# Kernel tuning notes

Measured on AMD Instinct MI355X. Metric: run time of the kernel, lower is better.

Reference implementation:

```python
import jax, jax.numpy as jnp
import numpy as np

N_NODES = 50000
N_EDGES = 1600000
IN_DIM = 128
HEADS = 4
HID = 16
NEG_SLOPE = 0.2  # DGL GATConv default


def setup_inputs() -> dict:
    key = jax.random.key(0)
    ks = jax.random.split(key, 7)
    features = jax.random.normal(ks[0], (N_NODES, IN_DIM), dtype=jnp.float32)
    W = jax.random.normal(ks[1], (IN_DIM, HEADS * HID), dtype=jnp.float32) * 0.1
    attn_l = jax.random.normal(ks[2], (HEADS, HID), dtype=jnp.float32) * 0.1
    attn_r = jax.random.normal(ks[3], (HEADS, HID), dtype=jnp.float32) * 0.1
    bias = jax.random.normal(ks[4], (HEADS * HID,), dtype=jnp.float32) * 0.1
    src = jax.random.randint(ks[5], (N_EDGES,), 0, N_NODES, dtype=jnp.int64)
    dst = jax.random.randint(ks[6], (N_EDGES,), 0, N_NODES, dtype=jnp.int64)
    return {"features": features, "W": W, "attn_l": attn_l, "attn_r": attn_r,
            "bias": bias, "src": src, "dst": dst}


def reference(features, W, attn_l, attn_r, bias, src, dst):
    N = features.shape[0]
    H, D = attn_l.shape
    # linear projection -> per-head features [N, H, D]
    feat = (features @ W).reshape(N, H, D)
    el = jnp.einsum('nhd,hd->nh', feat, attn_l)  # [N, H]
    er = jnp.einsum('nhd,hd->nh', feat, attn_r)  # [N, H]
    # per-edge unnormalized attention logits [E, H]
    e = jax.nn.leaky_relu(el[src] + er[dst], negative_slope=NEG_SLOPE)
    # edge softmax segmented by destination node (numerically stable)
    emax = jax.ops.segment_max(e, dst, num_segments=N)
    ee = jnp.exp(e - emax[dst])
    denom = jax.ops.segment_sum(ee, dst, num_segments=N)
    alpha = ee / denom[dst]  # [E, H]
    # weighted neighbor aggregation: scatter-add of alpha * feat[src]
    msg = feat[src] * alpha[:, :, None]  # [E, H, D]
    out = jax.ops.segment_sum(msg, dst, num_segments=N)  # [N, H, D]
    out = out + bias.reshape(1, H, D)
    # wrapper GAT.forward averages over heads
    return out.mean(axis=1)  # [N, D]
```

## Files before the change

### kernel.cpp

```cpp
#include <hip/hip_runtime.h>
#include <hip/hip_bf16.h>

#define IN_DIM 128
#define HEADS 4
#define HID 16
#define HD 64
#define NEG_SLOPE 0.2f
#define PSHIFT 7
#define PCAP 5120
#define NPMAX 512
#define EPB 4096

typedef __attribute__((ext_vector_type(8))) short bf16x8;
typedef __attribute__((ext_vector_type(4))) float f32x4;

__device__ __forceinline__ float lrelu_exp(float x) {
    float e = x > 0.0f ? x : NEG_SLOPE * x;
    return __expf(e);
}

__device__ __forceinline__ unsigned short f2bf(float x) {
    unsigned int u = __float_as_uint(x);
    return (unsigned short)((u + 0x7fffu + ((u >> 16) & 1u)) >> 16);
}

__global__ __launch_bounds__(256) void k_project(const float* __restrict__ features,
                                                 const float* __restrict__ W,
                                                 const float* __restrict__ attn_l,
                                                 const float* __restrict__ attn_r,
                                                 __hip_bfloat16* __restrict__ feat16,
                                                 float* __restrict__ el,
                                                 float* __restrict__ er,
                                                 int* __restrict__ cursor,
                                                 int n_nodes, int npart) {
    if (blockIdx.x == 0) {
        for (int i = threadIdx.x; i < npart; i += 256) cursor[i] = 0;
    }
    __shared__ float Wl[IN_DIM * HD];
    for (int i = threadIdx.x; i < IN_DIM * HD; i += 256) Wl[i] = W[i];
    __syncthreads();

    const int lane  = threadIdx.x & 63;
    const int wave  = threadIdx.x >> 6;
    const int colid = lane & 15;
    const int quad  = lane >> 4;

    float al[4], ar[4];
#pragma unroll
    for (int c = 0; c < 4; ++c) {
        al[c] = attn_l[c * 16 + colid];
        ar[c] = attn_r[c * 16 + colid];
    }

    bf16x8 bf[16];
#pragma unroll
    for (int c = 0; c < 4; ++c) {
#pragma unroll
        for (int q = 0; q < 4; ++q) {
            bf16x8 v;
#pragma unroll
            for (int j = 0; j < 8; ++j) {
                int k = q * 32 + quad * 8 + j;
                v[j] = (short)f2bf(Wl[k * HD + c * 16 + colid]);
            }
            bf[c * 4 + q] = v;
        }
    }

    const int ngroups = (n_nodes + 15) >> 4;
    const int gwave = blockIdx.x * 4 + wave;
    const int nwaves = gridDim.x * 4;

    for (int g = gwave; g < ngroups; g += nwaves) {
        const int n0 = g * 16;
        int rown = n0 + colid;
        if (rown >= n_nodes) rown = n_nodes - 1;
        const float* fp = features + (size_t)rown * IN_DIM + quad * 8;

        f32x4 acc0 = {0.f, 0.f, 0.f, 0.f};
        f32x4 acc1 = {0.f, 0.f, 0.f, 0.f};
        f32x4 acc2 = {0.f, 0.f, 0.f, 0.f};
        f32x4 acc3 = {0.f, 0.f, 0.f, 0.f};
#pragma unroll
        for (int q = 0; q < 4; ++q) {
            float4 a0 = *reinterpret_cast<const float4*>(fp + q * 32);
            float4 a1 = *reinterpret_cast<const float4*>(fp + q * 32 + 4);
            bf16x8 av;
            av[0] = (short)f2bf(a0.x); av[1] = (short)f2bf(a0.y);
            av[2] = (short)f2bf(a0.z); av[3] = (short)f2bf(a0.w);
            av[4] = (short)f2bf(a1.x); av[5] = (short)f2bf(a1.y);
            av[6] = (short)f2bf(a1.z); av[7] = (short)f2bf(a1.w);
            acc0 = __builtin_amdgcn_mfma_f32_16x16x32_bf16(av, bf[0 * 4 + q], acc0, 0, 0, 0);
            acc1 = __builtin_amdgcn_mfma_f32_16x16x32_bf16(av, bf[1 * 4 + q], acc1, 0, 0, 0);
            acc2 = __builtin_amdgcn_mfma_f32_16x16x32_bf16(av, bf[2 * 4 + q], acc2, 0, 0, 0);
            acc3 = __builtin_amdgcn_mfma_f32_16x16x32_bf16(av, bf[3 * 4 + q], acc3, 0, 0, 0);
        }

        f32x4 accs[4] = {acc0, acc1, acc2, acc3};
        const bool full = (n0 + 16 <= n_nodes);
#pragma unroll
        for (int c = 0; c < 4; ++c) {
            f32x4 v = accs[c];
#pragma unroll
            for (int r = 0; r < 4; ++r) {
                int n = n0 + quad * 4 + r;
                if (full || n < n_nodes) {
                    ((unsigned short*)feat16)[(size_t)n * HD + c * 16 + colid] = f2bf(v[r]);
                }
            }
            float pl0 = v[0] * al[c], pl1 = v[1] * al[c], pl2 = v[2] * al[c], pl3 = v[3] * al[c];
            float pr0 = v[0] * ar[c], pr1 = v[1] * ar[c], pr2 = v[2] * ar[c], pr3 = v[3] * ar[c];
#pragma unroll
            for (int m = 1; m < 16; m <<= 1) {
                pl0 += __shfl_xor(pl0, m); pl1 += __shfl_xor(pl1, m);
                pl2 += __shfl_xor(pl2, m); pl3 += __shfl_xor(pl3, m);
                pr0 += __shfl_xor(pr0, m); pr1 += __shfl_xor(pr1, m);
                pr2 += __shfl_xor(pr2, m); pr3 += __shfl_xor(pr3, m);
            }
            if (colid == 0) {
                int nb = n0 + quad * 4;
                if (full) {
                    el[(size_t)(nb + 0) * HEADS + c] = pl0;
                    el[(size_t)(nb + 1) * HEADS + c] = pl1;
                    el[(size_t)(nb + 2) * HEADS + c] = pl2;
                    el[(size_t)(nb + 3) * HEADS + c] = pl3;
                    er[(size_t)(nb + 0) * HEADS + c] = pr0;
                    er[(size_t)(nb + 1) * HEADS + c] = pr1;
                    er[(size_t)(nb + 2) * HEADS + c] = pr2;
                    er[(size_t)(nb + 3) * HEADS + c] = pr3;
                } else {
                    float pls[4] = {pl0, pl1, pl2, pl3};
                    float prs[4] = {pr0, pr1, pr2, pr3};
                    for (int r = 0; r < 4; ++r) {
                        if (nb + r < n_nodes) {
                            el[(size_t)(nb + r) * HEADS + c] = pls[r];
                            er[(size_t)(nb + r) * HEADS + c] = prs[r];
                        }
                    }
                }
            }
        }
    }
}

__global__ __launch_bounds__(256) void k_partition(const int* __restrict__ src,
                                                   const int* __restrict__ dst,
                                                   int* __restrict__ cursor,
                                                   unsigned int* __restrict__ partbuf,
                                                   int n_edges, int npart) {
    __shared__ int hist[NPMAX];
    __shared__ int base[NPMAX];
    const int t = threadIdx.x;
    for (int i = t; i < npart; i += 256) hist[i] = 0;
    __syncthreads();

    const int e0 = blockIdx.x * EPB;
    unsigned int vals[16];
#pragma unroll
    for (int j = 0; j < 4; ++j) {
        int e = e0 + j * 1024 + t * 4;
        if (e + 4 <= n_edges) {
            int4 s4 = *reinterpret_cast<const int4*>(src + e);
            int4 d4 = *reinterpret_cast<const int4*>(dst + e);
            vals[j * 4 + 0] = ((unsigned)d4.x << 16) | (unsigned)s4.x;
            vals[j * 4 + 1] = ((unsigned)d4.y << 16) | (unsigned)s4.y;
            vals[j * 4 + 2] = ((unsigned)d4.z << 16) | (unsigned)s4.z;
            vals[j * 4 + 3] = ((unsigned)d4.w << 16) | (unsigned)s4.w;
        } else {
#pragma unroll
            for (int k = 0; k < 4; ++k) {
                int ee = e + k;
                vals[j * 4 + k] = (ee < n_edges)
                    ? (((unsigned)dst[ee] << 16) | (unsigned)src[ee])
                    : 0xffffffffu;
            }
        }
    }
#pragma unroll
    for (int j = 0; j < 16; ++j)
        if (vals[j] != 0xffffffffu) atomicAdd(&hist[vals[j] >> (16 + PSHIFT)], 1);
    __syncthreads();
    for (int i = t; i < npart; i += 256) {
        base[i] = atomicAdd(&cursor[i], hist[i]);
        hist[i] = 0;
    }
    __syncthreads();
#pragma unroll
    for (int j = 0; j < 16; ++j) {
        unsigned int v = vals[j];
        if (v != 0xffffffffu) {
            int p = v >> (16 + PSHIFT);
            int idx = base[p] + atomicAdd(&hist[p], 1);
            if (idx < PCAP) partbuf[(size_t)p * PCAP + idx] = v;
        }
    }
}

__global__ __launch_bounds__(256) void k_sort(const unsigned int* __restrict__ partbuf,
                                              const int* __restrict__ cursor,
                                              unsigned short* __restrict__ csr,
                                              int* __restrict__ row_ptr,
                                              unsigned short* __restrict__ deg16,
                                              int n_nodes) {
    __shared__ int hist[128];
    __shared__ int scan_s[128];
    const int p = blockIdx.x;
    const int t = threadIdx.x;
    const int count = min(cursor[p], PCAP);
    const unsigned int* buf = partbuf + (size_t)p * PCAP;

    if (t < 128) hist[t] = 0;
    __syncthreads();
    for (int i = t; i < count; i += 256)
        atomicAdd(&hist[(buf[i] >> 16) & 127], 1);
    __syncthreads();

    int v = 0;
    if (t < 128) {
        v = hist[t];
        scan_s[t] = v;
    }
    __syncthreads();
    for (int off = 1; off < 128; off <<= 1) {
        int u = (t >= off && t < 128) ? scan_s[t - off] : 0;
        __syncthreads();
        if (t < 128) scan_s[t] += u;
        __syncthreads();
    }
    if (t < 128) {
        const int excl = scan_s[t] - v;
        const int node = (p << PSHIFT) + t;
        if (node < n_nodes) {
            row_ptr[node] = p * PCAP + excl;
            deg16[node] = (unsigned short)v;
        }
        hist[t] = excl;
    }
    __syncthreads();
    unsigned short* cbase = csr + (size_t)p * PCAP;
    for (int i = t; i < count; i += 256) {
        unsigned int val = buf[i];
        int ld = (val >> 16) & 127;
        int pos = atomicAdd(&hist[ld], 1);
        cbase[pos] = (unsigned short)(val & 0xffffu);
    }
}

__global__ __launch_bounds__(256) void k_agg(const int* __restrict__ row_ptr,
                                             const unsigned short* __restrict__ deg16,
                                             const unsigned short* __restrict__ csr,
                                             const float* __restrict__ el,
                                             const float* __restrict__ er,
                                             const unsigned int* __restrict__ feat16u,
                                             const float* __restrict__ bias,
                                             float* __restrict__ out,
                                             int n_nodes) {
    int n = (blockIdx.x * blockDim.x + threadIdx.x) >> 6;
    if (n >= n_nodes) return;
    const int lane = threadIdx.x & 63;
    const int half = lane >> 5;
    const int sub = lane & 31;
    const int h = sub >> 3;
    const int eW = lane >> 2;
    const int hW = lane & 3;

    const int beg = row_ptr[n];
    const int deg = (int)deg16[n];
    const unsigned short* row = csr + beg;
    const float erW = er[(size_t)n * HEADS + hW];

    const int baseLane = half * 4 + h;

    float nx0 = 0.f, ny0 = 0.f, nx1 = 0.f, ny1 = 0.f;
    float denacc = 0.f;

    for (int i0 = 0; i0 < deg; i0 += 16) {
        const int m = deg - i0;
        const bool valid = (eW < m);
        int s = valid ? (int)row[i0 + eW] : 0;
        float w = valid ? lrelu_exp(el[(size_t)s * HEADS + hW] + erW) : 0.f;
        denacc += w;
        const unsigned int pw = ((unsigned int)f2bf(w) << 16) | (unsigned int)s;

        unsigned int pk[8];
#pragma unroll
        for (int j = 0; j < 8; ++j) pk[j] = __shfl(pw, baseLane + (j << 3));
        unsigned int pf[8];
#pragma unroll
        for (int j = 0; j < 8; ++j)
            pf[j] = feat16u[((pk[j] & 0xffffu) << 5) + sub];
#pragma unroll
        for (int j = 0; j < 8; ++j) {
            float wj = __uint_as_float(pk[j] & 0xffff0000u);
            if (j & 1) {
                nx1 = fmaf(wj, __uint_as_float(pf[j] << 16), nx1);
                ny1 = fmaf(wj, __uint_as_float(pf[j] & 0xffff0000u), ny1);
            } else {
                nx0 = fmaf(wj, __uint_as_float(pf[j] << 16), nx0);
                ny0 = fmaf(wj, __uint_as_float(pf[j] & 0xffff0000u), ny0);
            }
        }
    }

    float den = denacc;
    den += __shfl_xor(den, 4);
    den += __shfl_xor(den, 8);
    den += __shfl_xor(den, 16);
    den += __shfl_xor(den, 32);
    float denh = __shfl(den, h);

    float nx = nx0 + nx1, ny = ny0 + ny1;
    nx += __shfl_xor(nx, 32);
    ny += __shfl_xor(ny, 32);
    float inv = (denh > 0.f) ? 0.25f / denh : 0.f;
    float rx = nx * inv;
    float ry = ny * inv;
    rx += __shfl_xor(rx, 8);
    ry += __shfl_xor(ry, 8);
    rx += __shfl_xor(rx, 16);
    ry += __shfl_xor(ry, 16);
    if (lane < 8) {
        int dp = lane;
        float bx = 0.25f * (bias[2 * dp] + bias[HID + 2 * dp] +
                            bias[2 * HID + 2 * dp] + bias[3 * HID + 2 * dp]);
        float by = 0.25f * (bias[2 * dp + 1] + bias[HID + 2 * dp + 1] +
                            bias[2 * HID + 2 * dp + 1] + bias[3 * HID + 2 * dp + 1]);
        *reinterpret_cast<float2*>(out + (size_t)n * HID + 2 * dp) =
            make_float2(rx + bx, ry + by);
    }
}

extern "C" void kernel_launch(void* const* d_in, const int* in_sizes, int n_in,
                              void* d_out, int out_size, void* d_ws, size_t ws_size,
                              hipStream_t stream) {
    const float* features = (const float*)d_in[0];
    const float* W        = (const float*)d_in[1];
    const float* attn_l   = (const float*)d_in[2];
    const float* attn_r   = (const float*)d_in[3];
    const float* bias     = (const float*)d_in[4];
    const int*   src      = (const int*)d_in[5];
    const int*   dst      = (const int*)d_in[6];
    float* out = (float*)d_out;

    const int n_nodes = in_sizes[0] / IN_DIM;
    const int n_edges = in_sizes[5];
    const int npart = (n_nodes + (1 << PSHIFT) - 1) >> PSHIFT;

    char* ws = (char*)d_ws;
    __hip_bfloat16* feat16 = (__hip_bfloat16*)ws; ws += (size_t)n_nodes * HD * sizeof(__hip_bfloat16);
    float* el      = (float*)ws;                  ws += (size_t)n_nodes * HEADS * sizeof(float);
    float* er      = (float*)ws;                  ws += (size_t)n_nodes * HEADS * sizeof(float);
    unsigned int* partbuf = (unsigned int*)ws;    ws += (size_t)npart * PCAP * sizeof(unsigned int);
    unsigned short* csr = (unsigned short*)ws;    ws += (size_t)npart * PCAP * sizeof(unsigned short);
    int* row_ptr   = (int*)ws;                    ws += (size_t)n_nodes * sizeof(int);
    unsigned short* deg16 = (unsigned short*)ws;  ws += (size_t)n_nodes * sizeof(unsigned short);
    int* cursor    = (int*)ws;                    ws += NPMAX * sizeof(int);

    k_project<<<768, 256, 0, stream>>>(features, W, attn_l, attn_r,
                                       feat16, el, er, cursor, n_nodes, npart);
    k_partition<<<(n_edges + EPB - 1) / EPB, 256, 0, stream>>>(src, dst, cursor,
                                                               partbuf, n_edges, npart);
    k_sort<<<npart, 256, 0, stream>>>(partbuf, cursor, csr, row_ptr, deg16, n_nodes);
    k_agg<<<(n_nodes + 3) / 4, 256, 0, stream>>>(row_ptr, deg16, csr, el, er,
                                                 (const unsigned int*)feat16, bias, out, n_nodes);
}
```

Baseline: 166.9 us.

## Fuse projection and edge partition kernels, register-cache sort input, unroll aggregation

Merges the projection and edge-partitioning kernels into one launch. The first blocks partition edges while the remaining blocks project features, sharing one shared-memory buffer, and the cursor reset moves to a memset. The sort kernel now loads its partition into registers once instead of reading it from global memory twice. The aggregation loop handles 32 edges per iteration instead of 16 to expose more independent gathers. The costs are higher register pressure, an extra memset launch, and a fixed cap of 20 loads per thread in the sort, which matches PCAP.

New measurement: 167.9 us. No clear change (+0.6%).

```diff
diff --git a/kernel.cpp b/kernel.cpp
--- a/kernel.cpp
+++ b/kernel.cpp
@@ -10,6 +10,7 @@
 #define PCAP 5120
 #define NPMAX 512
 #define EPB 4096
+#define NB_PROJ 768
 
 typedef __attribute__((ext_vector_type(8))) short bf16x8;
 typedef __attribute__((ext_vector_type(4))) float f32x4;
@@ -24,19 +25,72 @@
     return (unsigned short)((u + 0x7fffu + ((u >> 16) & 1u)) >> 16);
 }
 
-__global__ __launch_bounds__(256) void k_project(const float* __restrict__ features,
+__global__ __launch_bounds__(256) void k_prjpart(const float* __restrict__ features,
                                                  const float* __restrict__ W,
                                                  const float* __restrict__ attn_l,
                                                  const float* __restrict__ attn_r,
                                                  __hip_bfloat16* __restrict__ feat16,
                                                  float* __restrict__ el,
                                                  float* __restrict__ er,
+                                                 const int* __restrict__ src,
+                                                 const int* __restrict__ dst,
                                                  int* __restrict__ cursor,
-                                                 int n_nodes, int npart) {
-    if (blockIdx.x == 0) {
-        for (int i = threadIdx.x; i < npart; i += 256) cursor[i] = 0;
-    }
-    __shared__ float Wl[IN_DIM * HD];
+                                                 unsigned int* __restrict__ partbuf,
+                                                 int n_nodes, int n_edges,
+                                                 int npart, int npartblk) {
+    __shared__ float smem[IN_DIM * HD];
+
+    if (blockIdx.x < (unsigned)npartblk) {
+        int* hist = (int*)smem;
+        int* base = (int*)smem + NPMAX;
+        const int t = threadIdx.x;
+        for (int i = t; i < npart; i += 256) hist[i] = 0;
+        __syncthreads();
+
+        const int e0 = blockIdx.x * EPB;
+        unsigned int vals[16];
+#pragma unroll
+        for (int j = 0; j < 4; ++j) {
+            int e = e0 + j * 1024 + t * 4;
+            if (e + 4 <= n_edges) {
+                int4 s4 = *reinterpret_cast<const int4*>(src + e);
+                int4 d4 = *reinterpret_cast<const int4*>(dst + e);
+                vals[j * 4 + 0] = ((unsigned)d4.x << 16) | (unsigned)s4.x;
+                vals[j * 4 + 1] = ((unsigned)d4.y << 16) | (unsigned)s4.y;
+                vals[j * 4 + 2] = ((unsigned)d4.z << 16) | (unsigned)s4.z;
+                vals[j * 4 + 3] = ((unsigned)d4.w << 16) | (unsigned)s4.w;
+            } else {
+#pragma unroll
+                for (int k = 0; k < 4; ++k) {
+                    int ee = e + k;
+                    vals[j * 4 + k] = (ee < n_edges)
+                        ? (((unsigned)dst[ee] << 16) | (unsigned)src[ee])
+                        : 0xffffffffu;
+                }
+            }
+        }
+#pragma unroll
+        for (int j = 0; j < 16; ++j)
+            if (vals[j] != 0xffffffffu) atomicAdd(&hist[vals[j] >> (16 + PSHIFT)], 1);
+        __syncthreads();
+        for (int i = t; i < npart; i += 256) {
+            base[i] = atomicAdd(&cursor[i], hist[i]);
+            hist[i] = 0;
+        }
+        __syncthreads();
+#pragma unroll
+        for (int j = 0; j < 16; ++j) {
+            unsigned int v = vals[j];
+            if (v != 0xffffffffu) {
+                int p = v >> (16 + PSHIFT);
+                int idx = base[p] + atomicAdd(&hist[p], 1);
+                if (idx < PCAP) partbuf[(size_t)p * PCAP + idx] = v;
+            }
+        }
+        return;
+    }
+
+    float* Wl = smem;
     for (int i = threadIdx.x; i < IN_DIM * HD; i += 256) Wl[i] = W[i];
     __syncthreads();
 
@@ -68,8 +122,8 @@
     }
 
     const int ngroups = (n_nodes + 15) >> 4;
-    const int gwave = blockIdx.x * 4 + wave;
-    const int nwaves = gridDim.x * 4;
+    const int gwave = (blockIdx.x - npartblk) * 4 + wave;
+    const int nwaves = NB_PROJ * 4;
 
     for (int g = gwave; g < ngroups; g += nwaves) {
         const int n0 = g * 16;
@@ -143,59 +197,6 @@
     }
 }
 
-__global__ __launch_bounds__(256) void k_partition(const int* __restrict__ src,
-                                                   const int* __restrict__ dst,
-                                                   int* __restrict__ cursor,
-                                                   unsigned int* __restrict__ partbuf,
-                                                   int n_edges, int npart) {
-    __shared__ int hist[NPMAX];
-    __shared__ int base[NPMAX];
-    const int t = threadIdx.x;
-    for (int i = t; i < npart; i += 256) hist[i] = 0;
-    __syncthreads();
-
-    const int e0 = blockIdx.x * EPB;
-    unsigned int vals[16];
-#pragma unroll
-    for (int j = 0; j < 4; ++j) {
-        int e = e0 + j * 1024 + t * 4;
-        if (e + 4 <= n_edges) {
-            int4 s4 = *reinterpret_cast<const int4*>(src + e);
-            int4 d4 = *reinterpret_cast<const int4*>(dst + e);
-            vals[j * 4 + 0] = ((unsigned)d4.x << 16) | (unsigned)s4.x;
-            vals[j * 4 + 1] = ((unsigned)d4.y << 16) | (unsigned)s4.y;
-            vals[j * 4 + 2] = ((unsigned)d4.z << 16) | (unsigned)s4.z;
-            vals[j * 4 + 3] = ((unsigned)d4.w << 16) | (unsigned)s4.w;
-        } else {
-#pragma unroll
-            for (int k = 0; k < 4; ++k) {
-                int ee = e + k;
-                vals[j * 4 + k] = (ee < n_edges)
-                    ? (((unsigned)dst[ee] << 16) | (unsigned)src[ee])
-                    : 0xffffffffu;
-            }
-        }
-    }
-#pragma unroll
-    for (int j = 0; j < 16; ++j)
-        if (vals[j] != 0xffffffffu) atomicAdd(&hist[vals[j] >> (16 + PSHIFT)], 1);
-    __syncthreads();
-    for (int i = t; i < npart; i += 256) {
-        base[i] = atomicAdd(&cursor[i], hist[i]);
-        hist[i] = 0;
-    }
-    __syncthreads();
-#pragma unroll
-    for (int j = 0; j < 16; ++j) {
-        unsigned int v = vals[j];
-        if (v != 0xffffffffu) {
-            int p = v >> (16 + PSHIFT);
-            int idx = base[p] + atomicAdd(&hist[p], 1);
-            if (idx < PCAP) partbuf[(size_t)p * PCAP + idx] = v;
-        }
-    }
-}
-
 __global__ __launch_bounds__(256) void k_sort(const unsigned int* __restrict__ partbuf,
                                               const int* __restrict__ cursor,
                                               unsigned short* __restrict__ csr,
@@ -209,10 +210,18 @@
     const int count = min(cursor[p], PCAP);
     const unsigned int* buf = partbuf + (size_t)p * PCAP;
 
+    unsigned int vals[20];
+#pragma unroll
+    for (int j = 0; j < 20; ++j) {
+        int i = t + j * 256;
+        vals[j] = (i < count) ? buf[i] : 0xffffffffu;
+    }
+
     if (t < 128) hist[t] = 0;
     __syncthreads();
-    for (int i = t; i < count; i += 256)
-        atomicAdd(&hist[(buf[i] >> 16) & 127], 1);
+#pragma unroll
+    for (int j = 0; j < 20; ++j)
+        if (vals[j] != 0xffffffffu) atomicAdd(&hist[(vals[j] >> 16) & 127], 1);
     __syncthreads();
 
     int v = 0;
@@ -238,11 +247,14 @@
     }
     __syncthreads();
     unsigned short* cbase = csr + (size_t)p * PCAP;
-    for (int i = t; i < count; i += 256) {
-        unsigned int val = buf[i];
-        int ld = (val >> 16) & 127;
-        int pos = atomicAdd(&hist[ld], 1);
-        cbase[pos] = (unsigned short)(val & 0xffffu);
+#pragma unroll
+    for (int j = 0; j < 20; ++j) {
+        unsigned int val = vals[j];
+        if (val != 0xffffffffu) {
+            int ld = (val >> 16) & 127;
+            int pos = atomicAdd(&hist[ld], 1);
+            cbase[pos] = (unsigned short)(val & 0xffffu);
+        }
     }
 }
 
@@ -274,23 +286,30 @@
     float nx0 = 0.f, ny0 = 0.f, nx1 = 0.f, ny1 = 0.f;
     float denacc = 0.f;
 
-    for (int i0 = 0; i0 < deg; i0 += 16) {
+    for (int i0 = 0; i0 < deg; i0 += 32) {
         const int m = deg - i0;
-        const bool valid = (eW < m);
-        int s = valid ? (int)row[i0 + eW] : 0;
-        float w = valid ? lrelu_exp(el[(size_t)s * HEADS + hW] + erW) : 0.f;
-        denacc += w;
-        const unsigned int pw = ((unsigned int)f2bf(w) << 16) | (unsigned int)s;
-
-        unsigned int pk[8];
-#pragma unroll
-        for (int j = 0; j < 8; ++j) pk[j] = __shfl(pw, baseLane + (j << 3));
-        unsigned int pf[8];
-#pragma unroll
-        for (int j = 0; j < 8; ++j)
+        const bool v0 = (eW < m);
+        const bool v1 = (eW + 16 < m);
+        int s0 = v0 ? (int)row[i0 + eW] : 0;
+        int s1 = v1 ? (int)row[i0 + 16 + eW] : 0;
+        float w0 = v0 ? lrelu_exp(el[(size_t)s0 * HEADS + hW] + erW) : 0.f;
+        float w1 = v1 ? lrelu_exp(el[(size_t)s1 * HEADS + hW] + erW) : 0.f;
+        denacc += w0 + w1;
+        const unsigned int pw0 = ((unsigned int)f2bf(w0) << 16) | (unsigned int)s0;
+        const unsigned int pw1 = ((unsigned int)f2bf(w1) << 16) | (unsigned int)s1;
+
+        unsigned int pk[16];
+#pragma unroll
+        for (int j = 0; j < 8; ++j) {
+            pk[j]     = __shfl(pw0, baseLane + (j << 3));
+            pk[8 + j] = __shfl(pw1, baseLane + (j << 3));
+        }
+        unsigned int pf[16];
+#pragma unroll
+        for (int j = 0; j < 16; ++j)
             pf[j] = feat16u[((pk[j] & 0xffffu) << 5) + sub];
 #pragma unroll
-        for (int j = 0; j < 8; ++j) {
+        for (int j = 0; j < 16; ++j) {
             float wj = __uint_as_float(pk[j] & 0xffff0000u);
             if (j & 1) {
                 nx1 = fmaf(wj, __uint_as_float(pf[j] << 16), nx1);
@@ -345,6 +364,7 @@
     const int n_nodes = in_sizes[0] / IN_DIM;
     const int n_edges = in_sizes[5];
     const int npart = (n_nodes + (1 << PSHIFT) - 1) >> PSHIFT;
+    const int npartblk = (n_edges + EPB - 1) / EPB;
 
     char* ws = (char*)d_ws;
     __hip_bfloat16* feat16 = (__hip_bfloat16*)ws; ws += (size_t)n_nodes * HD * sizeof(__hip_bfloat16);
@@ -356,10 +376,12 @@
     unsigned short* deg16 = (unsigned short*)ws;  ws += (size_t)n_nodes * sizeof(unsigned short);
     int* cursor    = (int*)ws;                    ws += NPMAX * sizeof(int);
 
-    k_project<<<768, 256, 0, stream>>>(features, W, attn_l, attn_r,
-                                       feat16, el, er, cursor, n_nodes, npart);
-    k_partition<<<(n_edges + EPB - 1) / EPB, 256, 0, stream>>>(src, dst, cursor,
-                                                               partbuf, n_edges, npart);
+    hipMemsetAsync(cursor, 0, NPMAX * sizeof(int), stream);
+
+    k_prjpart<<<npartblk + NB_PROJ, 256, 0, stream>>>(features, W, attn_l, attn_r,
+                                                      feat16, el, er, src, dst,
+                                                      cursor, partbuf,
+                                                      n_nodes, n_edges, npart, npartblk);
     k_sort<<<npart, 256, 0, stream>>>(partbuf, cursor, csr, row_ptr, deg16, n_nodes);
     k_agg<<<(n_nodes + 3) / 4, 256, 0, stream>>>(row_ptr, deg16, csr, el, er,
                                                  (const unsigned int*)feat16, bias, out, n_nodes);
```
